# Optimization experiments

Hardware: AMD Instinct MI355X
Metric: run time of the kernel (lower is better)

The kernel has to match this reference:

```python
import jax, jax.numpy as jnp
import numpy as np

B = 256
DIM = 2048
H = W = 8
SLICE_MAX = 64
SLICE_RANGE = 2
TEMP = 0.1
BN_EPS = 1e-5
COS_EPS = 1e-8


def setup_inputs() -> dict:
    key = jax.random.key(0)
    ks = jax.random.split(key, 6)
    z0 = jax.random.normal(ks[0], (B, DIM, H, W), dtype=jnp.float32)
    z1 = jax.random.normal(ks[1], (B, DIM, H, W), dtype=jnp.float32)
    rel0 = jax.random.randint(ks[2], (B,), 0, SLICE_MAX)
    rel1 = jax.random.randint(ks[3], (B,), 0, SLICE_MAX)
    W1 = jax.random.normal(ks[4], (DIM, DIM), dtype=jnp.float32) * 0.02
    W2 = jax.random.normal(ks[5], (DIM, DIM), dtype=jnp.float32) * 0.02
    return {
        "z0": z0, "z1": z1,
        "rel_slice_idx_0": rel0, "rel_slice_idx_1": rel1,
        "W1": W1, "b1": jnp.zeros((DIM,), jnp.float32),
        "gamma": jnp.ones((DIM,), jnp.float32), "beta": jnp.zeros((DIM,), jnp.float32),
        "W2": W2, "b2": jnp.zeros((DIM,), jnp.float32),
    }


def _projection_head(z, W1, b1, gamma, beta, W2, b2):
    # AdaptiveAvgPool2d(1) + Flatten: [N, C, H, W] -> [N, C]
    p = jnp.mean(z, axis=(2, 3))
    h = p @ W1.T + b1
    # BatchNorm1d in training mode: batch statistics (biased variance)
    mu = jnp.mean(h, axis=0)
    var = jnp.var(h, axis=0)
    h = (h - mu) * jax.lax.rsqrt(var + BN_EPS) * gamma + beta
    h = jax.nn.relu(h)
    return h @ W2.T + b2


def reference(z0, z1, rel_slice_idx_0, rel_slice_idx_1, W1, b1, gamma, beta, W2, b2):
    # domain_contrast=True -> rel_slice_idx = rel_slice_idx_0 only
    rel = rel_slice_idx_0
    z = jnp.concatenate([z0, z1], axis=0)           # [2B, C, H, W]
    z = _projection_head(z, W1, b1, gamma, beta, W2, b2)  # [2B, DIM]

    # full cosine-similarity matrix (fused, instead of the per-row python loop)
    norms = jnp.maximum(jnp.linalg.norm(z, axis=1, keepdims=True), COS_EPS)
    zn = z / norms
    sim = zn @ zn.T                                  # [2B, 2B]
    # similarity_weighting='none' -> weights == 1
    S = jnp.exp(sim / TEMP)

    # relative-position pos/neg masks over the first B (same-domain) samples
    diff = jnp.abs(rel[:, None] - rel[None, :])      # [B, B]
    eye = jnp.eye(B, dtype=bool)
    pos_mask = (diff <= SLICE_RANGE) & (~eye)
    neg_mask = diff > SLICE_RANGE

    S_bb = S[:B, :B]
    # negatives = same-domain negatives + ALL other-domain samples (domain_contrast)
    neg_sum = jnp.sum(S_bb * neg_mask, axis=1) + jnp.sum(S[:B, B:], axis=1)  # [B]

    terms = -jnp.log(S_bb / (S_bb + neg_sum[:, None]))  # [B, B]
    cnt = jnp.sum(pos_mask, axis=1)
    loss_b = jnp.sum(terms * pos_mask, axis=1) / jnp.maximum(cnt, 1)
    defined = cnt > 0
    loss = jnp.sum(jnp.where(defined, loss_b, 0.0))
    n_defined = jnp.sum(defined)
    return loss, n_defined
```

## Files before the change

### kernel.cpp

```cpp
#include <hip/hip_runtime.h>

typedef __attribute__((ext_vector_type(8))) short s8v;
typedef __attribute__((ext_vector_type(4))) short s4v;
typedef __attribute__((ext_vector_type(4))) float f4v;

#define DIM 2048
#define NROW 512
#define NB 256

__device__ inline short f2bf(float f) {
    union { float f; unsigned int u; } v; v.f = f;
    unsigned int u = v.u;
    unsigned int r = (u + 0x7fffu + ((u >> 16) & 1u)) >> 16;
    return (short)r;
}

__device__ __forceinline__ int pk_trunc(float a, float b) {
    return __builtin_amdgcn_perm(__float_as_uint(b), __float_as_uint(a), 0x07060302);
}

__device__ __forceinline__ float qsum(float s) {
    int i = __float_as_int(s);
    s += __int_as_float(__builtin_amdgcn_update_dpp(i, i, 0xB1, 0xF, 0xF, false));
    i = __float_as_int(s);
    s += __int_as_float(__builtin_amdgcn_update_dpp(i, i, 0x4E, 0xF, 0xF, false));
    return s;
}

__global__ __launch_bounds__(256) void pool_kernel(const float* __restrict__ z0,
                                                   const float* __restrict__ z1,
                                                   short* __restrict__ p) {
    int t = threadIdx.x;
    int c = blockIdx.x;
    const float* src = (c < 4096) ? z0 + (long)c * 8192 : z1 + (long)(c - 4096) * 8192;
    int g = t >> 2, sub = t & 3;
    const float* base = src + g * 128 + sub * 4;
    f4v v[8];
#pragma unroll
    for (int j = 0; j < 8; ++j) v[j] = __builtin_nontemporal_load((const f4v*)(base + j * 16));
    float sA = 0.f, sB = 0.f;
#pragma unroll
    for (int j = 0; j < 4; ++j) sA += v[j].x + v[j].y + v[j].z + v[j].w;
#pragma unroll
    for (int j = 4; j < 8; ++j) sB += v[j].x + v[j].y + v[j].z + v[j].w;
    sA = qsum(sA);
    sB = qsum(sB);
    if (sub == 0) {
        int pk = (int)(unsigned short)f2bf(sA * (1.0f / 64.0f))
               | ((int)(unsigned short)f2bf(sB * (1.0f / 64.0f)) << 16);
        ((int*)p)[c * 64 + g] = pk;
    }
}

__global__ __launch_bounds__(256) void castw(const float* __restrict__ w,
                                             short* __restrict__ o) {
    int idx = (blockIdx.x * 256 + threadIdx.x) * 8;
    f4v x = __builtin_nontemporal_load((const f4v*)(w + idx));
    f4v y = __builtin_nontemporal_load((const f4v*)(w + idx + 4));
    int4 o4;
    o4.x = pk_trunc(x.x, x.y);
    o4.y = pk_trunc(x.z, x.w);
    o4.z = pk_trunc(y.x, y.y);
    o4.w = pk_trunc(y.z, y.w);
    *(int4*)(o + idx) = o4;
}

__device__ __forceinline__ int swz(int r, int k) { return r * 256 + (k ^ ((r & 7) << 3)); }

__global__ __launch_bounds__(256) void gemm_ks(const short* __restrict__ A,
                                               const short* __restrict__ Bh,
                                               const float* __restrict__ Bf,
                                               const float* __restrict__ bias,
                                               float* __restrict__ C,
                                               float* __restrict__ stats,
                                               int M, int N, int K, int kChunk) {
    __shared__ short sm[2 * 64 * 256];
    short* lA = sm;
    short* lB = sm + 64 * 256;
    int t = threadIdx.x;
    int n0 = blockIdx.x * 64, m0 = blockIdx.y * 64;
    int kbase = blockIdx.z * kChunk;
    long zoff = (long)blockIdx.z * M * N;
    int lane = t & 63, w = t >> 6;
    int l16 = lane & 15, quad = lane >> 4;
    int ks = w * 64;
    f4v acc[4][4] = {};
    int sr = t >> 3;
    int sq8 = (t & 7) * 8;

    for (int it = 0; it < kChunk; it += 256) {
        int k0 = kbase + it;
#pragma unroll
        for (int pp = 0; pp < 2; ++pp) {
            int r = sr + pp * 32;
            const short* as = &A[(long)(m0 + r) * K + k0];
#pragma unroll
            for (int j = 0; j < 4; ++j)
                *(s8v*)&lA[swz(r, sq8 + j * 64)] = *(const s8v*)&as[sq8 + j * 64];
        }
        if (Bh) {
#pragma unroll
            for (int pp = 0; pp < 2; ++pp) {
                int r = sr + pp * 32;
                const short* bs = &Bh[(long)(n0 + r) * K + k0];
#pragma unroll
                for (int j = 0; j < 4; ++j)
                    *(s8v*)&lB[swz(r, sq8 + j * 64)] = *(const s8v*)&bs[sq8 + j * 64];
            }
        } else {
#pragma unroll
            for (int pp = 0; pp < 2; ++pp) {
                int r = sr + pp * 32;
                const float* bs = &Bf[(long)(n0 + r) * K + k0];
#pragma unroll
                for (int j = 0; j < 4; ++j) {
                    float4 x = *(const float4*)&bs[sq8 + j * 64];
                    float4 y = *(const float4*)&bs[sq8 + j * 64 + 4];
                    int4 o;
                    o.x = pk_trunc(x.x, x.y);
                    o.y = pk_trunc(x.z, x.w);
                    o.z = pk_trunc(y.x, y.y);
                    o.w = pk_trunc(y.z, y.w);
                    *(int4*)&lB[swz(r, sq8 + j * 64)] = o;
                }
            }
        }
        __syncthreads();
#pragma unroll
        for (int kk = 0; kk < 2; ++kk) {
            s8v af[4], bf[4];
#pragma unroll
            for (int i = 0; i < 4; ++i)
                af[i] = *(const s8v*)&lA[swz(i * 16 + l16, ks + kk * 32 + quad * 8)];
#pragma unroll
            for (int j = 0; j < 4; ++j)
                bf[j] = *(const s8v*)&lB[swz(j * 16 + l16, ks + kk * 32 + quad * 8)];
#pragma unroll
            for (int i = 0; i < 4; ++i)
#pragma unroll
                for (int j = 0; j < 4; ++j)
                    acc[i][j] = __builtin_amdgcn_mfma_f32_16x16x32_bf16(af[i], bf[j], acc[i][j], 0, 0, 0);
        }
        __syncthreads();
    }

    float* fr = (float*)sm;
#pragma unroll
    for (int i = 0; i < 4; ++i)
#pragma unroll
        for (int j = 0; j < 4; ++j)
#pragma unroll
            for (int r = 0; r < 4; ++r)
                fr[w * 4096 + (i * 16 + quad * 4 + r) * 64 + j * 16 + l16] = acc[i][j][r];
    __syncthreads();
    int c = t & 63;
    int rbase = (t >> 6) * 16;
    float bv = bias ? bias[n0 + c] : 0.0f;
    float s = 0.f, q = 0.f;
#pragma unroll
    for (int r = 0; r < 16; ++r) {
        int rr = rbase + r;
        float h = fr[rr * 64 + c] + fr[4096 + rr * 64 + c]
                + fr[8192 + rr * 64 + c] + fr[12288 + rr * 64 + c] + bv;
        C[zoff + (long)(m0 + rr) * N + n0 + c] = h;
        s += h; q += h * h;
    }
    if (stats) {
        __syncthreads();
        fr[(t >> 6) * 64 + c] = s;
        fr[256 + (t >> 6) * 64 + c] = q;
        __syncthreads();
        if (t < 64) {
            float ss = fr[t] + fr[64 + t] + fr[128 + t] + fr[192 + t];
            float qq = fr[256 + t] + fr[320 + t] + fr[384 + t] + fr[448 + t];
            atomicAdd(&stats[n0 + t], ss);
            atomicAdd(&stats[2048 + n0 + t], qq);
        }
    }
}

__global__ __launch_bounds__(256) void bn_finalize(const float* __restrict__ stats,
                                                   const float* __restrict__ gamma,
                                                   const float* __restrict__ beta,
                                                   float* __restrict__ scale,
                                                   float* __restrict__ shift) {
    int c = blockIdx.x * 256 + threadIdx.x;
    float mu = stats[c] * (1.0f / NROW);
    float var = stats[2048 + c] * (1.0f / NROW) - mu * mu;
    float sc = gamma[c] * rsqrtf(var + 1e-5f);
    scale[c] = sc;
    shift[c] = beta[c] - mu * sc;
}

__global__ __launch_bounds__(256) void bn_relu_cast(const float* __restrict__ h,
                                                    const float* __restrict__ scale,
                                                    const float* __restrict__ shift,
                                                    short* __restrict__ hn) {
    int idx = (blockIdx.x * 256 + threadIdx.x) * 4;
    int col = idx & (DIM - 1);
    float4 v = *(const float4*)(h + idx);
    float4 sc = *(const float4*)(scale + col);
    float4 sh = *(const float4*)(shift + col);
    s4v o;
    o.x = f2bf(fmaxf(v.x * sc.x + sh.x, 0.f));
    o.y = f2bf(fmaxf(v.y * sc.y + sh.y, 0.f));
    o.z = f2bf(fmaxf(v.z * sc.z + sh.z, 0.f));
    o.w = f2bf(fmaxf(v.w * sc.w + sh.w, 0.f));
    *(s4v*)(hn + idx) = o;
}

__global__ __launch_bounds__(256) void rownorm(const float* __restrict__ z,
                                               short* __restrict__ zn) {
    __shared__ float red[4];
    int row = blockIdx.x, t = threadIdx.x;
    const float* zr = z + (long)row * DIM;
    float4 v0 = *(const float4*)(zr + t * 4);
    float4 v1 = *(const float4*)(zr + 1024 + t * 4);
    float ss = v0.x * v0.x + v0.y * v0.y + v0.z * v0.z + v0.w * v0.w
             + v1.x * v1.x + v1.y * v1.y + v1.z * v1.z + v1.w * v1.w;
#pragma unroll
    for (int m = 1; m < 64; m <<= 1) ss += __shfl_xor(ss, m);
    if ((t & 63) == 0) red[t >> 6] = ss;
    __syncthreads();
    float tot = red[0] + red[1] + red[2] + red[3];
    float inv = 1.0f / fmaxf(sqrtf(tot), 1e-8f);
    s4v a, b;
    a.x = f2bf(v0.x * inv); a.y = f2bf(v0.y * inv); a.z = f2bf(v0.z * inv); a.w = f2bf(v0.w * inv);
    b.x = f2bf(v1.x * inv); b.y = f2bf(v1.y * inv); b.z = f2bf(v1.z * inv); b.w = f2bf(v1.w * inv);
    *(s4v*)(zn + (long)row * DIM + t * 4) = a;
    *(s4v*)(zn + (long)row * DIM + 1024 + t * 4) = b;
}

__global__ __launch_bounds__(256) void ksum8(const float* __restrict__ simp,
                                             float* __restrict__ sim,
                                             float* __restrict__ out) {
    int idx = (blockIdx.x * 256 + threadIdx.x) * 4;
    float4 o = {0.f, 0.f, 0.f, 0.f};
#pragma unroll
    for (int z = 0; z < 8; ++z) {
        float4 a = *(const float4*)(simp + (long)z * 131072 + idx);
        o.x += a.x; o.y += a.y; o.z += a.z; o.w += a.w;
    }
    *(float4*)(sim + idx) = o;
    if (blockIdx.x == 0 && threadIdx.x == 0) { out[0] = 0.f; out[1] = 0.f; }
}

__global__ __launch_bounds__(256) void loss_kernel(const float* __restrict__ sim,
                                                   const int* __restrict__ rel,
                                                   float* __restrict__ out) {
    __shared__ float lsum[4];
    __shared__ float lcnt[4];
    int t = threadIdx.x, lane = t & 63, wave = t >> 6;
    int i = blockIdx.x * 4 + wave;
    int reli = rel[i];
    float s[8];
    float neg = 0.f;
#pragma unroll
    for (int kk = 0; kk < 8; ++kk) {
        int j = lane + kk * 64;
        s[kk] = sim[i * 512 + j];
        float e = __expf(10.0f * s[kk]);
        if (j >= NB || abs(reli - rel[j]) > 2) neg += e;
    }
#pragma unroll
    for (int m = 1; m < 64; m <<= 1) neg += __shfl_xor(neg, m);
    float ts = 0.f; int cnt = 0;
#pragma unroll
    for (int kk = 0; kk < 4; ++kk) {
        int j = lane + kk * 64;
        if (j != i && abs(reli - rel[j]) <= 2) {
            ts += logf(__expf(10.0f * s[kk]) + neg) - 10.0f * s[kk];
            cnt++;
        }
    }
#pragma unroll
    for (int m = 1; m < 64; m <<= 1) {
        ts += __shfl_xor(ts, m);
        cnt += __shfl_xor(cnt, m);
    }
    if (lane == 0) {
        lsum[wave] = (cnt > 0) ? ts / (float)cnt : 0.f;
        lcnt[wave] = (cnt > 0) ? 1.f : 0.f;
    }
    __syncthreads();
    if (t == 0) {
        atomicAdd(&out[0], lsum[0] + lsum[1] + lsum[2] + lsum[3]);
        atomicAdd(&out[1], lcnt[0] + lcnt[1] + lcnt[2] + lcnt[3]);
    }
}

extern "C" void kernel_launch(void* const* d_in, const int* in_sizes, int n_in,
                              void* d_out, int out_size, void* d_ws, size_t ws_size,
                              hipStream_t stream) {
    const float* z0    = (const float*)d_in[0];
    const float* z1    = (const float*)d_in[1];
    const int*   rel0  = (const int*)d_in[2];
    const float* W1    = (const float*)d_in[4];
    const float* b1    = (const float*)d_in[5];
    const float* gamma = (const float*)d_in[6];
    const float* beta  = (const float*)d_in[7];
    const float* W2    = (const float*)d_in[8];
    const float* b2    = (const float*)d_in[9];

    char* ws = (char*)d_ws;
    short* p_bf  = (short*)(ws);
    float* h     = (float*)(ws + (2l  << 20));
    short* hn    = (short*)(ws + (6l  << 20));
    float* zproj = (float*)(ws + (8l  << 20));
    short* zn    = (short*)(ws + (12l << 20));
    float* simp  = (float*)(ws + (14l << 20));
    float* sim   = (float*)(ws + (18l << 20));
    float* stats = (float*)(ws + (19l << 20));
    float* scale = (float*)(ws + (19l << 20) + 16384);
    float* shift = (float*)(ws + (19l << 20) + 24576);
    short* w1h   = (short*)(ws + (20l << 20));
    short* w2h   = (short*)(ws + (28l << 20));
    bool castok = ws_size >= (36l << 20);

    hipMemsetAsync(stats, 0, 16384, stream);
    if (castok) {
        castw<<<2048, 256, 0, stream>>>(W1, w1h);
        castw<<<2048, 256, 0, stream>>>(W2, w2h);
    }
    pool_kernel<<<8192, 256, 0, stream>>>(z0, z1, p_bf);
    gemm_ks<<<dim3(32, 8, 1), 256, 0, stream>>>(p_bf, castok ? w1h : nullptr,
                                                castok ? nullptr : W1, b1, h, stats,
                                                NROW, DIM, DIM, DIM);
    bn_finalize<<<8, 256, 0, stream>>>(stats, gamma, beta, scale, shift);
    bn_relu_cast<<<1024, 256, 0, stream>>>(h, scale, shift, hn);
    gemm_ks<<<dim3(32, 8, 1), 256, 0, stream>>>(hn, castok ? w2h : nullptr,
                                                castok ? nullptr : W2, b2, zproj, nullptr,
                                                NROW, DIM, DIM, DIM);
    rownorm<<<512, 256, 0, stream>>>(zproj, zn);
    gemm_ks<<<dim3(8, 4, 8), 256, 0, stream>>>(zn, zn, nullptr, nullptr, simp, nullptr,
                                               NB, NROW, DIM, 256);
    ksum8<<<128, 256, 0, stream>>>(simp, sim, (float*)d_out);
    loss_kernel<<<64, 256, 0, stream>>>(sim, rel0, (float*)d_out);
}
```

Before: 340.5 us.

## Fuse small kernels: pool+cast+memset, BN finalize into apply, ksum into loss

Merges the weight casts, the stats memset and the pooling into one launch. BN finalize is folded into the bn_relu_cast elementwise kernel, and the split-K reduction is folded into a per-row loss kernel, which drops the intermediate sim buffer and several launches. The output zeroing moves into rownorm. This cuts launch overhead and inter-kernel gaps. In exchange, the per-element rsqrt in the BN apply is recomputed for every row, and the loss kernel now spreads its work over more blocks.

```diff
diff --git a/kernel.cpp b/kernel.cpp
--- a/kernel.cpp
+++ b/kernel.cpp
@@ -27,42 +27,54 @@
     return s;
 }
 
-__global__ __launch_bounds__(256) void pool_kernel(const float* __restrict__ z0,
-                                                   const float* __restrict__ z1,
-                                                   short* __restrict__ p) {
+__global__ __launch_bounds__(256) void pool_cast(const float* __restrict__ z0,
+                                                 const float* __restrict__ z1,
+                                                 const float* __restrict__ W1,
+                                                 const float* __restrict__ W2,
+                                                 short* __restrict__ p,
+                                                 short* __restrict__ w1h,
+                                                 short* __restrict__ w2h,
+                                                 float* __restrict__ stats) {
     int t = threadIdx.x;
     int c = blockIdx.x;
-    const float* src = (c < 4096) ? z0 + (long)c * 8192 : z1 + (long)(c - 4096) * 8192;
-    int g = t >> 2, sub = t & 3;
-    const float* base = src + g * 128 + sub * 4;
-    f4v v[8];
-#pragma unroll
-    for (int j = 0; j < 8; ++j) v[j] = __builtin_nontemporal_load((const f4v*)(base + j * 16));
-    float sA = 0.f, sB = 0.f;
-#pragma unroll
-    for (int j = 0; j < 4; ++j) sA += v[j].x + v[j].y + v[j].z + v[j].w;
-#pragma unroll
-    for (int j = 4; j < 8; ++j) sB += v[j].x + v[j].y + v[j].z + v[j].w;
-    sA = qsum(sA);
-    sB = qsum(sB);
-    if (sub == 0) {
-        int pk = (int)(unsigned short)f2bf(sA * (1.0f / 64.0f))
-               | ((int)(unsigned short)f2bf(sB * (1.0f / 64.0f)) << 16);
-        ((int*)p)[c * 64 + g] = pk;
-    }
-}
-
-__global__ __launch_bounds__(256) void castw(const float* __restrict__ w,
-                                             short* __restrict__ o) {
-    int idx = (blockIdx.x * 256 + threadIdx.x) * 8;
-    f4v x = __builtin_nontemporal_load((const f4v*)(w + idx));
-    f4v y = __builtin_nontemporal_load((const f4v*)(w + idx + 4));
-    int4 o4;
-    o4.x = pk_trunc(x.x, x.y);
-    o4.y = pk_trunc(x.z, x.w);
-    o4.z = pk_trunc(y.x, y.y);
-    o4.w = pk_trunc(y.z, y.w);
-    *(int4*)(o + idx) = o4;
+    if (c < 8192) {
+        const float* src = (c < 4096) ? z0 + (long)c * 8192 : z1 + (long)(c - 4096) * 8192;
+        int g = t >> 2, sub = t & 3;
+        const float* base = src + g * 128 + sub * 4;
+        f4v v[8];
+#pragma unroll
+        for (int j = 0; j < 8; ++j) v[j] = __builtin_nontemporal_load((const f4v*)(base + j * 16));
+        __builtin_amdgcn_sched_barrier(0);
+        float sA = 0.f, sB = 0.f;
+#pragma unroll
+        for (int j = 0; j < 4; ++j) sA += v[j].x + v[j].y + v[j].z + v[j].w;
+#pragma unroll
+        for (int j = 4; j < 8; ++j) sB += v[j].x + v[j].y + v[j].z + v[j].w;
+        sA = qsum(sA);
+        sB = qsum(sB);
+        if (sub == 0) {
+            int pk = (int)(unsigned short)f2bf(sA * (1.0f / 64.0f))
+                   | ((int)(unsigned short)f2bf(sB * (1.0f / 64.0f)) << 16);
+            ((int*)p)[c * 64 + g] = pk;
+        }
+    } else {
+        int cc = c - 8192;
+        const float* w = (cc < 2048) ? W1 : W2;
+        short* o = (cc < 2048) ? w1h : w2h;
+        int idx = (cc & 2047) * 2048 + t * 8;
+        f4v x = __builtin_nontemporal_load((const f4v*)(w + idx));
+        f4v y = __builtin_nontemporal_load((const f4v*)(w + idx + 4));
+        int4 o4;
+        o4.x = pk_trunc(x.x, x.y);
+        o4.y = pk_trunc(x.z, x.w);
+        o4.z = pk_trunc(y.x, y.y);
+        o4.w = pk_trunc(y.z, y.w);
+        *(int4*)(o + idx) = o4;
+        if (cc == 0) {
+#pragma unroll
+            for (int k = 0; k < 16; ++k) stats[t + k * 256] = 0.f;
+        }
+    }
 }
 
 __device__ __forceinline__ int swz(int r, int k) { return r * 256 + (k ^ ((r & 7) << 3)); }
@@ -179,40 +191,41 @@
     }
 }
 
-__global__ __launch_bounds__(256) void bn_finalize(const float* __restrict__ stats,
-                                                   const float* __restrict__ gamma,
-                                                   const float* __restrict__ beta,
-                                                   float* __restrict__ scale,
-                                                   float* __restrict__ shift) {
-    int c = blockIdx.x * 256 + threadIdx.x;
-    float mu = stats[c] * (1.0f / NROW);
-    float var = stats[2048 + c] * (1.0f / NROW) - mu * mu;
-    float sc = gamma[c] * rsqrtf(var + 1e-5f);
-    scale[c] = sc;
-    shift[c] = beta[c] - mu * sc;
-}
-
 __global__ __launch_bounds__(256) void bn_relu_cast(const float* __restrict__ h,
-                                                    const float* __restrict__ scale,
-                                                    const float* __restrict__ shift,
+                                                    const float* __restrict__ stats,
+                                                    const float* __restrict__ gamma,
+                                                    const float* __restrict__ beta,
                                                     short* __restrict__ hn) {
     int idx = (blockIdx.x * 256 + threadIdx.x) * 4;
     int col = idx & (DIM - 1);
-    float4 v = *(const float4*)(h + idx);
-    float4 sc = *(const float4*)(scale + col);
-    float4 sh = *(const float4*)(shift + col);
+    float4 s0 = *(const float4*)(stats + col);
+    float4 s1 = *(const float4*)(stats + 2048 + col);
+    float4 g  = *(const float4*)(gamma + col);
+    float4 bt = *(const float4*)(beta + col);
+    float4 v  = *(const float4*)(h + idx);
+    float mu, var, sc, sh;
     s4v o;
-    o.x = f2bf(fmaxf(v.x * sc.x + sh.x, 0.f));
-    o.y = f2bf(fmaxf(v.y * sc.y + sh.y, 0.f));
-    o.z = f2bf(fmaxf(v.z * sc.z + sh.z, 0.f));
-    o.w = f2bf(fmaxf(v.w * sc.w + sh.w, 0.f));
+    mu = s0.x * (1.0f / NROW); var = s1.x * (1.0f / NROW) - mu * mu;
+    sc = g.x * rsqrtf(var + 1e-5f); sh = bt.x - mu * sc;
+    o.x = f2bf(fmaxf(v.x * sc + sh, 0.f));
+    mu = s0.y * (1.0f / NROW); var = s1.y * (1.0f / NROW) - mu * mu;
+    sc = g.y * rsqrtf(var + 1e-5f); sh = bt.y - mu * sc;
+    o.y = f2bf(fmaxf(v.y * sc + sh, 0.f));
+    mu = s0.z * (1.0f / NROW); var = s1.z * (1.0f / NROW) - mu * mu;
+    sc = g.z * rsqrtf(var + 1e-5f); sh = bt.z - mu * sc;
+    o.z = f2bf(fmaxf(v.z * sc + sh, 0.f));
+    mu = s0.w * (1.0f / NROW); var = s1.w * (1.0f / NROW) - mu * mu;
+    sc = g.w * rsqrtf(var + 1e-5f); sh = bt.w - mu * sc;
+    o.w = f2bf(fmaxf(v.w * sc + sh, 0.f));
     *(s4v*)(hn + idx) = o;
 }
 
 __global__ __launch_bounds__(256) void rownorm(const float* __restrict__ z,
-                                               short* __restrict__ zn) {
+                                               short* __restrict__ zn,
+                                               float* __restrict__ out) {
     __shared__ float red[4];
     int row = blockIdx.x, t = threadIdx.x;
+    if (row == 0 && t == 0) { out[0] = 0.f; out[1] = 0.f; }
     const float* zr = z + (long)row * DIM;
     float4 v0 = *(const float4*)(zr + t * 4);
     float4 v1 = *(const float4*)(zr + 1024 + t * 4);
@@ -231,61 +244,38 @@
     *(s4v*)(zn + (long)row * DIM + 1024 + t * 4) = b;
 }
 
-__global__ __launch_bounds__(256) void ksum8(const float* __restrict__ simp,
-                                             float* __restrict__ sim,
-                                             float* __restrict__ out) {
-    int idx = (blockIdx.x * 256 + threadIdx.x) * 4;
-    float4 o = {0.f, 0.f, 0.f, 0.f};
+__global__ __launch_bounds__(256) void loss_fused(const float* __restrict__ simp,
+                                                  const int* __restrict__ rel,
+                                                  float* __restrict__ out) {
+    __shared__ float red[4], rts[4], rct[4];
+    int i = blockIdx.x, t = threadIdx.x, lane = t & 63, wave = t >> 6;
+    int reli = rel[i];
+    float s0 = 0.f, s1 = 0.f;
 #pragma unroll
     for (int z = 0; z < 8; ++z) {
-        float4 a = *(const float4*)(simp + (long)z * 131072 + idx);
-        o.x += a.x; o.y += a.y; o.z += a.z; o.w += a.w;
-    }
-    *(float4*)(sim + idx) = o;
-    if (blockIdx.x == 0 && threadIdx.x == 0) { out[0] = 0.f; out[1] = 0.f; }
-}
-
-__global__ __launch_bounds__(256) void loss_kernel(const float* __restrict__ sim,
-                                                   const int* __restrict__ rel,
-                                                   float* __restrict__ out) {
-    __shared__ float lsum[4];
-    __shared__ float lcnt[4];
-    int t = threadIdx.x, lane = t & 63, wave = t >> 6;
-    int i = blockIdx.x * 4 + wave;
-    int reli = rel[i];
-    float s[8];
-    float neg = 0.f;
-#pragma unroll
-    for (int kk = 0; kk < 8; ++kk) {
-        int j = lane + kk * 64;
-        s[kk] = sim[i * 512 + j];
-        float e = __expf(10.0f * s[kk]);
-        if (j >= NB || abs(reli - rel[j]) > 2) neg += e;
-    }
+        s0 += simp[(long)z * 131072 + i * 512 + t];
+        s1 += simp[(long)z * 131072 + i * 512 + 256 + t];
+    }
+    float e0 = __expf(10.0f * s0);
+    float e1 = __expf(10.0f * s1);
+    int d = abs(reli - rel[t]);
+    float neg = e1 + ((d > 2) ? e0 : 0.f);
 #pragma unroll
     for (int m = 1; m < 64; m <<= 1) neg += __shfl_xor(neg, m);
-    float ts = 0.f; int cnt = 0;
-#pragma unroll
-    for (int kk = 0; kk < 4; ++kk) {
-        int j = lane + kk * 64;
-        if (j != i && abs(reli - rel[j]) <= 2) {
-            ts += logf(__expf(10.0f * s[kk]) + neg) - 10.0f * s[kk];
-            cnt++;
-        }
-    }
-#pragma unroll
-    for (int m = 1; m < 64; m <<= 1) {
-        ts += __shfl_xor(ts, m);
-        cnt += __shfl_xor(cnt, m);
-    }
-    if (lane == 0) {
-        lsum[wave] = (cnt > 0) ? ts / (float)cnt : 0.f;
-        lcnt[wave] = (cnt > 0) ? 1.f : 0.f;
-    }
+    if (lane == 0) red[wave] = neg;
+    __syncthreads();
+    neg = red[0] + red[1] + red[2] + red[3];
+    float ts = 0.f, cnt = 0.f;
+    if (t != i && d <= 2) { ts = logf(e0 + neg) - 10.0f * s0; cnt = 1.f; }
+#pragma unroll
+    for (int m = 1; m < 64; m <<= 1) { ts += __shfl_xor(ts, m); cnt += __shfl_xor(cnt, m); }
+    if (lane == 0) { rts[wave] = ts; rct[wave] = cnt; }
     __syncthreads();
     if (t == 0) {
-        atomicAdd(&out[0], lsum[0] + lsum[1] + lsum[2] + lsum[3]);
-        atomicAdd(&out[1], lcnt[0] + lcnt[1] + lcnt[2] + lcnt[3]);
+        float T = rts[0] + rts[1] + rts[2] + rts[3];
+        float C = rct[0] + rct[1] + rct[2] + rct[3];
+        atomicAdd(&out[0], C > 0.f ? T / C : 0.f);
+        atomicAdd(&out[1], C > 0.f ? 1.f : 0.f);
     }
 }
 
@@ -309,31 +299,27 @@
     float* zproj = (float*)(ws + (8l  << 20));
     short* zn    = (short*)(ws + (12l << 20));
     float* simp  = (float*)(ws + (14l << 20));
-    float* sim   = (float*)(ws + (18l << 20));
     float* stats = (float*)(ws + (19l << 20));
-    float* scale = (float*)(ws + (19l << 20) + 16384);
-    float* shift = (float*)(ws + (19l << 20) + 24576);
     short* w1h   = (short*)(ws + (20l << 20));
     short* w2h   = (short*)(ws + (28l << 20));
     bool castok = ws_size >= (36l << 20);
 
-    hipMemsetAsync(stats, 0, 16384, stream);
     if (castok) {
-        castw<<<2048, 256, 0, stream>>>(W1, w1h);
-        castw<<<2048, 256, 0, stream>>>(W2, w2h);
-    }
-    pool_kernel<<<8192, 256, 0, stream>>>(z0, z1, p_bf);
+        pool_cast<<<12288, 256, 0, stream>>>(z0, z1, W1, W2, p_bf, w1h, w2h, stats);
+    } else {
+        hipMemsetAsync(stats, 0, 16384, stream);
+        pool_cast<<<8192, 256, 0, stream>>>(z0, z1, nullptr, nullptr, p_bf,
+                                            nullptr, nullptr, nullptr);
+    }
     gemm_ks<<<dim3(32, 8, 1), 256, 0, stream>>>(p_bf, castok ? w1h : nullptr,
                                                 castok ? nullptr : W1, b1, h, stats,
                                                 NROW, DIM, DIM, DIM);
-    bn_finalize<<<8, 256, 0, stream>>>(stats, gamma, beta, scale, shift);
-    bn_relu_cast<<<1024, 256, 0, stream>>>(h, scale, shift, hn);
+    bn_relu_cast<<<1024, 256, 0, stream>>>(h, stats, gamma, beta, hn);
     gemm_ks<<<dim3(32, 8, 1), 256, 0, stream>>>(hn, castok ? w2h : nullptr,
                                                 castok ? nullptr : W2, b2, zproj, nullptr,
                                                 NROW, DIM, DIM, DIM);
-    rownorm<<<512, 256, 0, stream>>>(zproj, zn);
+    rownorm<<<512, 256, 0, stream>>>(zproj, zn, (float*)d_out);
     gemm_ks<<<dim3(8, 4, 8), 256, 0, stream>>>(zn, zn, nullptr, nullptr, simp, nullptr,
                                                NB, NROW, DIM, 256);
-    ksum8<<<128, 256, 0, stream>>>(simp, sim, (float*)d_out);
-    loss_kernel<<<64, 256, 0, stream>>>(sim, rel0, (float*)d_out);
-}
+    loss_fused<<<NB, 256, 0, stream>>>(simp, rel0, (float*)d_out);
+}
```

After: 337.1 us. Within noise of the previous version (-1.0%).
